# Kernel optimization log

Hardware: AMD Instinct MI355X
Metric: run time of the kernel (lower is better)

Reference implementation:

```python
import jax, jax.numpy as jnp
import numpy as np

DIM = 512
BATCH = 65536


def setup_inputs() -> dict:
    key = jax.random.key(0)
    k1, k2 = jax.random.split(key)
    pq = jax.random.normal(k1, (BATCH, 2 * DIM), dtype=jnp.float32)
    A = jax.random.normal(k2, (DIM, DIM), dtype=jnp.float32)
    return {"pq": pq, "A": A}


def reference(pq, A):
    # up_or_low == 'up': pterm_i = (A + A^T) @ q_i, qterm = 0
    # npq = [p + pterm, q]
    S = A + A.T  # symmetric (dim, dim)
    p = pq[:, :DIM]
    q = pq[:, DIM:]
    # torch.mv(S, q_i) for every row i  ==  q @ S.T  (single batched matvec/GEMM)
    pterm = jnp.einsum("bd,ed->be", q, S)
    return jnp.concatenate([p + pterm, q], axis=-1)
```

## Files before the change

kernel.cpp:

```cpp
#include <hip/hip_runtime.h>

#define DIM 512
#define BATCH 65536
#define BM 32
#define THREADS 512

typedef float f32x4 __attribute__((ext_vector_type(4)));
typedef float f32x16 __attribute__((ext_vector_type(16)));
typedef __bf16 bf16x8 __attribute__((ext_vector_type(8)));

__device__ __forceinline__ unsigned f2bf(float f) {
    unsigned u = __float_as_uint(f);
    return (u + 0x7FFFu + ((u >> 16) & 1u)) >> 16;
}

__global__ void prep_Sfrag(const float* __restrict__ A, unsigned short* __restrict__ Sf) {
    int idx = blockIdx.x * 256 + threadIdx.x;
    int lane = idx & 63;
    int np   = (idx >> 6) & 15;
    int k0   = idx >> 10;
    int n     = np * 32 + (lane & 31);
    int kbase = k0 * 16 + (lane >> 5) * 8;
    unsigned short tmp[8];
    #pragma unroll
    for (int j = 0; j < 8; ++j) {
        int k = kbase + j;
        tmp[j] = (unsigned short)f2bf(A[n * DIM + k] + A[k * DIM + n]);
    }
    *(uint4*)(Sf + (size_t)idx * 8) = *(const uint4*)tmp;
}

__global__ __launch_bounds__(THREADS, 4)
void gemm_kernel(const float* __restrict__ pq,
                 const unsigned short* __restrict__ Sf,
                 float* __restrict__ out) {
    __shared__ unsigned short qs[BM * DIM];
    const int b0 = blockIdx.x * BM;
    const int tid = threadIdx.x;

    #pragma unroll
    for (int i = 0; i < 8; ++i) {
        int flat = (tid + i * THREADS) * 4;
        int r = flat >> 9;
        int c = flat & 511;
        const size_t g = (size_t)(b0 + r) * 1024 + 512 + c;
        f32x4 v = *(const f32x4*)(pq + g);
        *(f32x4*)(out + g) = v;
        unsigned lo = f2bf(v.x) | (f2bf(v.y) << 16);
        unsigned hi = f2bf(v.z) | (f2bf(v.w) << 16);
        int byteoff = (c * 2) ^ ((r & 15) << 4);
        *(uint2*)((char*)qs + r * 1024 + byteoff) = make_uint2(lo, hi);
    }
    __syncthreads();

    const int wid  = tid >> 6;
    const int lane = tid & 63;
    const int row  = lane & 31;
    const int kphase = (lane >> 5) * 16;

    const unsigned short* Sfp = Sf + ((size_t)(wid * 2) * 64 + lane) * 8;

    f32x16 acc0 = {}, acc1 = {};
    #pragma unroll 4
    for (int k0 = 0; k0 < 32; ++k0) {
        int byteoff = (k0 * 32 + kphase) ^ ((row & 15) << 4);
        bf16x8 a   = *(const bf16x8*)((const char*)qs + row * 1024 + byteoff);
        bf16x8 bv0 = *(const bf16x8*)(Sfp + (size_t)k0 * 8192);
        bf16x8 bv1 = *(const bf16x8*)(Sfp + (size_t)k0 * 8192 + 512);
        acc0 = __builtin_amdgcn_mfma_f32_32x32x16_bf16(a, bv0, acc0, 0, 0, 0);
        acc1 = __builtin_amdgcn_mfma_f32_32x32x16_bf16(a, bv1, acc1, 0, 0, 0);
    }

    const int col0 = wid * 64 + row;
    const int rsub = 4 * (lane >> 5);
    #pragma unroll
    for (int reg = 0; reg < 16; ++reg) {
        int r = (reg & 3) + 8 * (reg >> 2) + rsub;
        size_t g = (size_t)(b0 + r) * 1024;
        out[g + col0 +  0] = pq[g + col0 +  0] + acc0[reg];
        out[g + col0 + 32] = pq[g + col0 + 32] + acc1[reg];
    }
}

extern "C" void kernel_launch(void* const* d_in, const int* in_sizes, int n_in,
                              void* d_out, int out_size, void* d_ws, size_t ws_size,
                              hipStream_t stream) {
    const float* pq = (const float*)d_in[0];
    const float* A  = (const float*)d_in[1];
    float* out = (float*)d_out;
    unsigned short* Sf = (unsigned short*)d_ws;

    prep_Sfrag<<<128, 256, 0, stream>>>(A, Sf);
    gemm_kernel<<<BATCH / BM, THREADS, 0, stream>>>(pq, Sf, out);
}
```

Before: 160.2 us.

## Process four row tiles per block with double-buffered LDS and prefetching

Each block now handles four 32-row tiles instead of one. The next tile's q values are loaded into registers while the current tile's MFMA loop runs, then written into a second LDS buffer, and the p values for the epilogue are loaded before the compute. The k-loop is fully unrolled with register prefetch of the A and B fragments. The aim is to hide global memory latency behind compute and amortise launch and setup cost, at the price of more registers, fewer resident blocks (launch bounds 4 to 2), and a grid of only 512 blocks.

After: 343.8 us. 2.15x slower.

```diff
diff --git a/kernel.cpp b/kernel.cpp
--- a/kernel.cpp
+++ b/kernel.cpp
@@ -4,6 +4,8 @@
 #define BATCH 65536
 #define BM 32
 #define THREADS 512
+#define TILES 4
+#define NBLK (BATCH / (BM * TILES))
 
 typedef float f32x4 __attribute__((ext_vector_type(4)));
 typedef float f32x16 __attribute__((ext_vector_type(16)));
@@ -30,55 +32,101 @@
     *(uint4*)(Sf + (size_t)idx * 8) = *(const uint4*)tmp;
 }
 
-__global__ __launch_bounds__(THREADS, 4)
+__global__ __launch_bounds__(THREADS, 2)
 void gemm_kernel(const float* __restrict__ pq,
                  const unsigned short* __restrict__ Sf,
                  float* __restrict__ out) {
-    __shared__ unsigned short qs[BM * DIM];
-    const int b0 = blockIdx.x * BM;
-    const int tid = threadIdx.x;
+    __shared__ unsigned short qs[2][BM * DIM];
+    const int tid  = threadIdx.x;
+    const int wid  = tid >> 6;
+    const int lane = tid & 63;
+    const int row  = lane & 31;
+    const int khalf = lane >> 5;
+    const size_t brow0 = (size_t)blockIdx.x * (BM * TILES);
 
     #pragma unroll
-    for (int i = 0; i < 8; ++i) {
-        int flat = (tid + i * THREADS) * 4;
-        int r = flat >> 9;
-        int c = flat & 511;
-        const size_t g = (size_t)(b0 + r) * 1024 + 512 + c;
+    for (int j = 0; j < 8; ++j) {
+        int flat = (tid + j * THREADS) * 4;
+        int r = flat >> 9, c = flat & 511;
+        size_t g = (brow0 + r) * 1024 + 512 + c;
         f32x4 v = *(const f32x4*)(pq + g);
         *(f32x4*)(out + g) = v;
         unsigned lo = f2bf(v.x) | (f2bf(v.y) << 16);
         unsigned hi = f2bf(v.z) | (f2bf(v.w) << 16);
-        int byteoff = (c * 2) ^ ((r & 15) << 4);
-        *(uint2*)((char*)qs + r * 1024 + byteoff) = make_uint2(lo, hi);
+        int bo = (c * 2) ^ ((r & 15) << 4);
+        *(uint2*)((char*)qs[0] + r * 1024 + bo) = make_uint2(lo, hi);
     }
     __syncthreads();
 
-    const int wid  = tid >> 6;
-    const int lane = tid & 63;
-    const int row  = lane & 31;
-    const int kphase = (lane >> 5) * 16;
+    const unsigned short* Sfp = Sf + ((size_t)(wid * 2) * 64 + lane) * 8;
+    const int col0 = wid * 64 + row;
+    const int rsub = 4 * khalf;
 
-    const unsigned short* Sfp = Sf + ((size_t)(wid * 2) * 64 + lane) * 8;
+    for (int t = 0; t < TILES; ++t) {
+        const size_t trow0 = brow0 + (size_t)t * BM;
+        const unsigned short* qb = qs[t & 1];
 
-    f32x16 acc0 = {}, acc1 = {};
-    #pragma unroll 4
-    for (int k0 = 0; k0 < 32; ++k0) {
-        int byteoff = (k0 * 32 + kphase) ^ ((row & 15) << 4);
-        bf16x8 a   = *(const bf16x8*)((const char*)qs + row * 1024 + byteoff);
-        bf16x8 bv0 = *(const bf16x8*)(Sfp + (size_t)k0 * 8192);
-        bf16x8 bv1 = *(const bf16x8*)(Sfp + (size_t)k0 * 8192 + 512);
-        acc0 = __builtin_amdgcn_mfma_f32_32x32x16_bf16(a, bv0, acc0, 0, 0, 0);
-        acc1 = __builtin_amdgcn_mfma_f32_32x32x16_bf16(a, bv1, acc1, 0, 0, 0);
-    }
+        f32x4 nv[8];
+        if (t + 1 < TILES) {
+            #pragma unroll
+            for (int j = 0; j < 8; ++j) {
+                int flat = (tid + j * THREADS) * 4;
+                int r = flat >> 9, c = flat & 511;
+                size_t g = (trow0 + BM + r) * 1024 + 512 + c;
+                nv[j] = *(const f32x4*)(pq + g);
+            }
+        }
+        float pv0[16], pv1[16];
+        #pragma unroll
+        for (int reg = 0; reg < 16; ++reg) {
+            int r = (reg & 3) + 8 * (reg >> 2) + rsub;
+            size_t g = (trow0 + r) * 1024;
+            pv0[reg] = pq[g + col0];
+            pv1[reg] = pq[g + col0 + 32];
+        }
 
-    const int col0 = wid * 64 + row;
-    const int rsub = 4 * (lane >> 5);
-    #pragma unroll
-    for (int reg = 0; reg < 16; ++reg) {
-        int r = (reg & 3) + 8 * (reg >> 2) + rsub;
-        size_t g = (size_t)(b0 + r) * 1024;
-        out[g + col0 +  0] = pq[g + col0 +  0] + acc0[reg];
-        out[g + col0 + 32] = pq[g + col0 + 32] + acc1[reg];
+        f32x16 acc0 = {}, acc1 = {};
+        bf16x8 a_c  = *(const bf16x8*)((const char*)qb + row * 1024 +
+                                       ((khalf * 16) ^ ((row & 15) << 4)));
+        bf16x8 b0_c = *(const bf16x8*)(Sfp);
+        bf16x8 b1_c = *(const bf16x8*)(Sfp + 512);
+        #pragma unroll
+        for (int k0 = 0; k0 < 32; ++k0) {
+            bf16x8 a_n, b0_n, b1_n;
+            if (k0 < 31) {
+                int bo = ((k0 + 1) * 32 + khalf * 16) ^ ((row & 15) << 4);
+                a_n  = *(const bf16x8*)((const char*)qb + row * 1024 + bo);
+                b0_n = *(const bf16x8*)(Sfp + (size_t)(k0 + 1) * 8192);
+                b1_n = *(const bf16x8*)(Sfp + (size_t)(k0 + 1) * 8192 + 512);
+            }
+            acc0 = __builtin_amdgcn_mfma_f32_32x32x16_bf16(a_c, b0_c, acc0, 0, 0, 0);
+            acc1 = __builtin_amdgcn_mfma_f32_32x32x16_bf16(a_c, b1_c, acc1, 0, 0, 0);
+            if (k0 < 31) { a_c = a_n; b0_c = b0_n; b1_c = b1_n; }
+        }
+
+        #pragma unroll
+        for (int reg = 0; reg < 16; ++reg) {
+            int r = (reg & 3) + 8 * (reg >> 2) + rsub;
+            size_t g = (trow0 + r) * 1024;
+            out[g + col0]      = pv0[reg] + acc0[reg];
+            out[g + col0 + 32] = pv1[reg] + acc1[reg];
+        }
+
+        if (t + 1 < TILES) {
+            unsigned short* qn = qs[(t + 1) & 1];
+            #pragma unroll
+            for (int j = 0; j < 8; ++j) {
+                int flat = (tid + j * THREADS) * 4;
+                int r = flat >> 9, c = flat & 511;
+                size_t g = (trow0 + BM + r) * 1024 + 512 + c;
+                *(f32x4*)(out + g) = nv[j];
+                unsigned lo = f2bf(nv[j].x) | (f2bf(nv[j].y) << 16);
+                unsigned hi = f2bf(nv[j].z) | (f2bf(nv[j].w) << 16);
+                int bo = (c * 2) ^ ((r & 15) << 4);
+                *(uint2*)((char*)qn + r * 1024 + bo) = make_uint2(lo, hi);
+            }
+        }
+        __syncthreads();
     }
 }
 
@@ -91,5 +139,5 @@
     unsigned short* Sf = (unsigned short*)d_ws;
 
     prep_Sfrag<<<128, 256, 0, stream>>>(A, Sf);
-    gemm_kernel<<<BATCH / BM, THREADS, 0, stream>>>(pq, Sf, out);
+    gemm_kernel<<<NBLK, THREADS, 0, stream>>>(pq, Sf, out);
 }
```

## Stage GEMM epilogue through LDS for vectorized stores, prefetch operands, nontemporal IO

Applied to the files above, without the earlier changes.

The accumulator epilogue now writes results to shared memory and reads them back so each thread does 16-byte coalesced loads of p and 16-byte stores of the output, replacing scattered scalar accesses. The k-loop is fully unrolled with register double-buffering of the A and B fragments, so the next fragment is loaded while the current MFMAs issue. Global loads and stores of pq/out use nontemporal hints to limit cache pollution. The cost is extra LDS traffic and three more block barriers per tile.

Result: faster. 135.2 us (-15.6%).

```diff
diff --git a/kernel.cpp b/kernel.cpp
--- a/kernel.cpp
+++ b/kernel.cpp
@@ -35,50 +35,69 @@
                  const unsigned short* __restrict__ Sf,
                  float* __restrict__ out) {
     __shared__ unsigned short qs[BM * DIM];
-    const int b0 = blockIdx.x * BM;
+    const int rb  = blockIdx.x * BM;
     const int tid = threadIdx.x;
+    const int wid  = tid >> 6;
+    const int lane = tid & 63;
+    const int row  = lane & 31;
+    const int khalf = lane >> 5;
 
     #pragma unroll
     for (int i = 0; i < 8; ++i) {
         int flat = (tid + i * THREADS) * 4;
-        int r = flat >> 9;
-        int c = flat & 511;
-        const size_t g = (size_t)(b0 + r) * 1024 + 512 + c;
-        f32x4 v = *(const f32x4*)(pq + g);
-        *(f32x4*)(out + g) = v;
+        int r = flat >> 9, c = flat & 511;
+        size_t g = (size_t)(rb + r) * 1024 + 512 + c;
+        f32x4 v = __builtin_nontemporal_load((const f32x4*)(pq + g));
+        __builtin_nontemporal_store(v, (f32x4*)(out + g));
         unsigned lo = f2bf(v.x) | (f2bf(v.y) << 16);
         unsigned hi = f2bf(v.z) | (f2bf(v.w) << 16);
-        int byteoff = (c * 2) ^ ((r & 15) << 4);
-        *(uint2*)((char*)qs + r * 1024 + byteoff) = make_uint2(lo, hi);
+        int bo = (c * 2) ^ ((r & 15) << 4);
+        *(uint2*)((char*)qs + r * 1024 + bo) = make_uint2(lo, hi);
     }
     __syncthreads();
 
-    const int wid  = tid >> 6;
-    const int lane = tid & 63;
-    const int row  = lane & 31;
-    const int kphase = (lane >> 5) * 16;
-
     const unsigned short* Sfp = Sf + ((size_t)(wid * 2) * 64 + lane) * 8;
-
     f32x16 acc0 = {}, acc1 = {};
-    #pragma unroll 4
+    bf16x8 a_c  = *(const bf16x8*)((const char*)qs + row * 1024 +
+                                   ((khalf * 16) ^ ((row & 15) << 4)));
+    bf16x8 b0_c = *(const bf16x8*)(Sfp);
+    bf16x8 b1_c = *(const bf16x8*)(Sfp + 512);
+    #pragma unroll
     for (int k0 = 0; k0 < 32; ++k0) {
-        int byteoff = (k0 * 32 + kphase) ^ ((row & 15) << 4);
-        bf16x8 a   = *(const bf16x8*)((const char*)qs + row * 1024 + byteoff);
-        bf16x8 bv0 = *(const bf16x8*)(Sfp + (size_t)k0 * 8192);
-        bf16x8 bv1 = *(const bf16x8*)(Sfp + (size_t)k0 * 8192 + 512);
-        acc0 = __builtin_amdgcn_mfma_f32_32x32x16_bf16(a, bv0, acc0, 0, 0, 0);
-        acc1 = __builtin_amdgcn_mfma_f32_32x32x16_bf16(a, bv1, acc1, 0, 0, 0);
+        bf16x8 a_n, b0_n, b1_n;
+        if (k0 < 31) {
+            int bo = ((k0 + 1) * 32 + khalf * 16) ^ ((row & 15) << 4);
+            a_n  = *(const bf16x8*)((const char*)qs + row * 1024 + bo);
+            b0_n = *(const bf16x8*)(Sfp + (size_t)(k0 + 1) * 8192);
+            b1_n = *(const bf16x8*)(Sfp + (size_t)(k0 + 1) * 8192 + 512);
+        }
+        acc0 = __builtin_amdgcn_mfma_f32_32x32x16_bf16(a_c, b0_c, acc0, 0, 0, 0);
+        acc1 = __builtin_amdgcn_mfma_f32_32x32x16_bf16(a_c, b1_c, acc1, 0, 0, 0);
+        if (k0 < 31) { a_c = a_n; b0_c = b0_n; b1_c = b1_n; }
     }
 
-    const int col0 = wid * 64 + row;
-    const int rsub = 4 * (lane >> 5);
+    float* sc = (float*)qs;
+    __syncthreads();
     #pragma unroll
-    for (int reg = 0; reg < 16; ++reg) {
-        int r = (reg & 3) + 8 * (reg >> 2) + rsub;
-        size_t g = (size_t)(b0 + r) * 1024;
-        out[g + col0 +  0] = pq[g + col0 +  0] + acc0[reg];
-        out[g + col0 + 32] = pq[g + col0 + 32] + acc1[reg];
+    for (int pass = 0; pass < 2; ++pass) {
+        const f32x16& ac = pass ? acc1 : acc0;
+        #pragma unroll
+        for (int reg = 0; reg < 16; ++reg) {
+            int r = (reg & 3) + 8 * (reg >> 2) + 4 * khalf;
+            sc[r * 256 + wid * 32 + row] = ac[reg];
+        }
+        __syncthreads();
+        #pragma unroll
+        for (int j = 0; j < 4; ++j) {
+            int c  = tid + j * 512;
+            int r  = c >> 6, cc = c & 63;
+            int gcol = (cc >> 3) * 64 + (cc & 7) * 4 + pass * 32;
+            size_t g = (size_t)(rb + r) * 1024 + gcol;
+            f32x4 v  = *(const f32x4*)(sc + r * 256 + cc * 4);
+            f32x4 pv = __builtin_nontemporal_load((const f32x4*)(pq + g));
+            __builtin_nontemporal_store(pv + v, (f32x4*)(out + g));
+        }
+        __syncthreads();
     }
 }
 
```

## Pipeline q loads across K-halves and tiles with LDS-staged coalesced epilogue

Applied to the files above, without the earlier changes.

Each block now handles four 32-row tiles. It splits K into two halves with double-buffered bf16 q tiles in LDS, so global loads of the next half or tile overlap the MFMA work on the current one. The epilogue stages accumulators through shared memory, so p loads and output stores become coalesced 16-byte nontemporal accesses, and B fragments are software-prefetched one step ahead. In exchange it adds more __syncthreads, more LDS (which may lower occupancy), and a quarter as many blocks.

Result: slower. 374.8 us (+134.0%).

```diff
diff --git a/kernel.cpp b/kernel.cpp
--- a/kernel.cpp
+++ b/kernel.cpp
@@ -4,6 +4,8 @@
 #define BATCH 65536
 #define BM 32
 #define THREADS 512
+#define TILES 4
+#define NBLK (BATCH / (BM * TILES))
 
 typedef float f32x4 __attribute__((ext_vector_type(4)));
 typedef float f32x16 __attribute__((ext_vector_type(16)));
@@ -34,51 +36,120 @@
 void gemm_kernel(const float* __restrict__ pq,
                  const unsigned short* __restrict__ Sf,
                  float* __restrict__ out) {
-    __shared__ unsigned short qs[BM * DIM];
-    const int b0 = blockIdx.x * BM;
-    const int tid = threadIdx.x;
-
-    #pragma unroll
-    for (int i = 0; i < 8; ++i) {
-        int flat = (tid + i * THREADS) * 4;
-        int r = flat >> 9;
-        int c = flat & 511;
-        const size_t g = (size_t)(b0 + r) * 1024 + 512 + c;
-        f32x4 v = *(const f32x4*)(pq + g);
-        *(f32x4*)(out + g) = v;
-        unsigned lo = f2bf(v.x) | (f2bf(v.y) << 16);
-        unsigned hi = f2bf(v.z) | (f2bf(v.w) << 16);
-        int byteoff = (c * 2) ^ ((r & 15) << 4);
-        *(uint2*)((char*)qs + r * 1024 + byteoff) = make_uint2(lo, hi);
-    }
-    __syncthreads();
-
+    __shared__ __align__(16) unsigned short qh0[BM * 256];
+    __shared__ __align__(16) unsigned short qh1[BM * 256];
+    __shared__ float sc[BM * 256];
+    const int tid  = threadIdx.x;
     const int wid  = tid >> 6;
     const int lane = tid & 63;
     const int row  = lane & 31;
-    const int kphase = (lane >> 5) * 16;
-
+    const int khalf = lane >> 5;
+    const int rb = blockIdx.x * (BM * TILES);
     const unsigned short* Sfp = Sf + ((size_t)(wid * 2) * 64 + lane) * 8;
 
-    f32x16 acc0 = {}, acc1 = {};
-    #pragma unroll 4
-    for (int k0 = 0; k0 < 32; ++k0) {
-        int byteoff = (k0 * 32 + kphase) ^ ((row & 15) << 4);
-        bf16x8 a   = *(const bf16x8*)((const char*)qs + row * 1024 + byteoff);
-        bf16x8 bv0 = *(const bf16x8*)(Sfp + (size_t)k0 * 8192);
-        bf16x8 bv1 = *(const bf16x8*)(Sfp + (size_t)k0 * 8192 + 512);
-        acc0 = __builtin_amdgcn_mfma_f32_32x32x16_bf16(a, bv0, acc0, 0, 0, 0);
-        acc1 = __builtin_amdgcn_mfma_f32_32x32x16_bf16(a, bv1, acc1, 0, 0, 0);
-    }
+    const int r0 = tid >> 5,              c80 = tid & 31;
+    const int r1 = (THREADS + tid) >> 5,  c81 = tid & 31;
+    const int wbo0 = r0 * 512 + ((c80 * 16) ^ ((r0 & 7) << 4));
+    const int wbo1 = r1 * 512 + ((c81 * 16) ^ ((r1 & 7) << 4));
 
-    const int col0 = wid * 64 + row;
-    const int rsub = 4 * (lane >> 5);
-    #pragma unroll
-    for (int reg = 0; reg < 16; ++reg) {
-        int r = (reg & 3) + 8 * (reg >> 2) + rsub;
-        size_t g = (size_t)(b0 + r) * 1024;
-        out[g + col0 +  0] = pq[g + col0 +  0] + acc0[reg];
-        out[g + col0 + 32] = pq[g + col0 + 32] + acc1[reg];
+    f32x4 stg0, stg1, stg2, stg3;
+    f32x4 pv0, pv1, pv2, pv3, pv4, pv5, pv6, pv7;
+    f32x16 acc0, acc1;
+
+#define Q_OFF(tile, half, rr, cc8) \
+    ((size_t)(rb + (tile) * BM + (rr)) * 1024 + 512 + (half) * 256 + (cc8) * 8)
+
+#define ISSUE_Q(tile, half) do { \
+    stg0 = __builtin_nontemporal_load((const f32x4*)(pq + Q_OFF(tile, half, r0, c80)));     \
+    stg1 = __builtin_nontemporal_load((const f32x4*)(pq + Q_OFF(tile, half, r0, c80) + 4)); \
+    stg2 = __builtin_nontemporal_load((const f32x4*)(pq + Q_OFF(tile, half, r1, c81)));     \
+    stg3 = __builtin_nontemporal_load((const f32x4*)(pq + Q_OFF(tile, half, r1, c81) + 4)); \
+} while (0)
+
+#define WRITE_BACK(tile, half, dst) do { \
+    size_t g0_ = Q_OFF(tile, half, r0, c80), g1_ = Q_OFF(tile, half, r1, c81); \
+    __builtin_nontemporal_store(stg0, (f32x4*)(out + g0_));     \
+    __builtin_nontemporal_store(stg1, (f32x4*)(out + g0_ + 4)); \
+    __builtin_nontemporal_store(stg2, (f32x4*)(out + g1_));     \
+    __builtin_nontemporal_store(stg3, (f32x4*)(out + g1_ + 4)); \
+    *(uint4*)((char*)(dst) + wbo0) = make_uint4( \
+        f2bf(stg0.x) | (f2bf(stg0.y) << 16), f2bf(stg0.z) | (f2bf(stg0.w) << 16), \
+        f2bf(stg1.x) | (f2bf(stg1.y) << 16), f2bf(stg1.z) | (f2bf(stg1.w) << 16)); \
+    *(uint4*)((char*)(dst) + wbo1) = make_uint4( \
+        f2bf(stg2.x) | (f2bf(stg2.y) << 16), f2bf(stg2.z) | (f2bf(stg2.w) << 16), \
+        f2bf(stg3.x) | (f2bf(stg3.y) << 16), f2bf(stg3.z) | (f2bf(stg3.w) << 16)); \
+} while (0)
+
+#define EJ(j)    (tid + (j) * 512)
+#define EROW(j)  (EJ(j) >> 6)
+#define ECC(j)   (EJ(j) & 63)
+#define EGCOL(j) (((ECC(j) >> 3) * 64) + ((ECC(j) & 7) * 4))
+#define ESCO(j)  (EROW(j) * 256 + ECC(j) * 4)
+#define P_OFF(tb, j, pass) ((size_t)((tb) + EROW(j)) * 1024 + EGCOL(j) + (pass) * 32)
+
+#define PREFETCH_P(tile) do { int tb_ = rb + (tile) * BM; \
+    pv0 = __builtin_nontemporal_load((const f32x4*)(pq + P_OFF(tb_, 0, 0))); \
+    pv1 = __builtin_nontemporal_load((const f32x4*)(pq + P_OFF(tb_, 1, 0))); \
+    pv2 = __builtin_nontemporal_load((const f32x4*)(pq + P_OFF(tb_, 2, 0))); \
+    pv3 = __builtin_nontemporal_load((const f32x4*)(pq + P_OFF(tb_, 3, 0))); \
+    pv4 = __builtin_nontemporal_load((const f32x4*)(pq + P_OFF(tb_, 0, 1))); \
+    pv5 = __builtin_nontemporal_load((const f32x4*)(pq + P_OFF(tb_, 1, 1))); \
+    pv6 = __builtin_nontemporal_load((const f32x4*)(pq + P_OFF(tb_, 2, 1))); \
+    pv7 = __builtin_nontemporal_load((const f32x4*)(pq + P_OFF(tb_, 3, 1))); \
+} while (0)
+
+#define KHALF(buf, half) do { \
+    const unsigned short* sp_ = Sfp + (size_t)(half) * 16 * 8192; \
+    bf16x8 b0c = *(const bf16x8*)(sp_);       \
+    bf16x8 b1c = *(const bf16x8*)(sp_ + 512); \
+    _Pragma("unroll") \
+    for (int k = 0; k < 16; ++k) { \
+        bf16x8 b0n, b1n; \
+        if (k < 15) { \
+            b0n = *(const bf16x8*)(sp_ + (size_t)(k + 1) * 8192);       \
+            b1n = *(const bf16x8*)(sp_ + (size_t)(k + 1) * 8192 + 512); \
+        } \
+        int bo_ = row * 512 + ((k * 32 + khalf * 16) ^ ((row & 7) << 4)); \
+        bf16x8 a_ = *(const bf16x8*)((const char*)(buf) + bo_); \
+        acc0 = __builtin_amdgcn_mfma_f32_32x32x16_bf16(a_, b0c, acc0, 0, 0, 0); \
+        acc1 = __builtin_amdgcn_mfma_f32_32x32x16_bf16(a_, b1c, acc1, 0, 0, 0); \
+        if (k < 15) { b0c = b0n; b1c = b1n; } \
+    } \
+} while (0)
+
+#define EPI_PASS(tb, ac, pA, pB, pC, pD, pass) do { \
+    _Pragma("unroll") \
+    for (int reg = 0; reg < 16; ++reg) { \
+        int r_ = (reg & 3) + 8 * (reg >> 2) + 4 * khalf; \
+        sc[r_ * 256 + wid * 32 + row] = (ac)[reg];    \
+    } \
+    __syncthreads(); \
+    __builtin_nontemporal_store((pA) + *(const f32x4*)(sc + ESCO(0)), (f32x4*)(out + P_OFF(tb, 0, pass))); \
+    __builtin_nontemporal_store((pB) + *(const f32x4*)(sc + ESCO(1)), (f32x4*)(out + P_OFF(tb, 1, pass))); \
+    __builtin_nontemporal_store((pC) + *(const f32x4*)(sc + ESCO(2)), (f32x4*)(out + P_OFF(tb, 2, pass))); \
+    __builtin_nontemporal_store((pD) + *(const f32x4*)(sc + ESCO(3)), (f32x4*)(out + P_OFF(tb, 3, pass))); \
+    __syncthreads(); \
+} while (0)
+
+    ISSUE_Q(0, 0);
+    WRITE_BACK(0, 0, qh0);
+    __syncthreads();
+
+    for (int t = 0; t < TILES; ++t) {
+        acc0 = f32x16{};
+        acc1 = f32x16{};
+        PREFETCH_P(t);
+        ISSUE_Q(t, 1);
+        KHALF(qh0, 0);
+        WRITE_BACK(t, 1, qh1);
+        __syncthreads();
+        if (t + 1 < TILES) ISSUE_Q(t + 1, 0);
+        KHALF(qh1, 1);
+        if (t + 1 < TILES) WRITE_BACK(t + 1, 0, qh0);
+        __syncthreads();
+        int tb = rb + t * BM;
+        EPI_PASS(tb, acc0, pv0, pv1, pv2, pv3, 0);
+        EPI_PASS(tb, acc1, pv4, pv5, pv6, pv7, 1);
     }
 }
 
@@ -91,5 +162,5 @@
     unsigned short* Sf = (unsigned short*)d_ws;
 
     prep_Sfrag<<<128, 256, 0, stream>>>(A, Sf);
-    gemm_kernel<<<BATCH / BM, THREADS, 0, stream>>>(pq, Sf, out);
+    gemm_kernel<<<NBLK, THREADS, 0, stream>>>(pq, Sf, out);
 }
```
